# Optimization experiments

Measured on AMD Instinct MI355X. Metric: run time of the kernel, lower is better.

## Reference

```python
import jax, jax.numpy as jnp
import numpy as np

B, N, C_IN, C_OUT, D, K = 64, 2048, 32, 32, 16, 2


def setup_inputs() -> dict:
    key = jax.random.key(0)
    k1, k2, k3, k4 = jax.random.split(key, 4)
    x = jax.random.normal(k1, (B, N, C_IN), dtype=jnp.float32)
    node_embeddings = jax.random.normal(k2, (N, D), dtype=jnp.float32)
    weights_pool = jax.random.normal(k3, (D, K, C_IN, C_OUT), dtype=jnp.float32)
    bias_pool = jax.random.normal(k4, (D, C_OUT), dtype=jnp.float32)
    return {"x": x, "node_embeddings": node_embeddings,
            "weights_pool": weights_pool, "bias_pool": bias_pool}


def reference(x, node_embeddings, weights_pool, bias_pool):
    n = node_embeddings.shape[0]
    # adaptive adjacency: softmax(relu(E E^T), axis=1)  [N, N]
    supports = jax.nn.softmax(jax.nn.relu(node_embeddings @ node_embeddings.T), axis=1)
    # stack [I, A]  -> [K=2, N, N]
    supports = jnp.stack([jnp.eye(n, dtype=supports.dtype), supports], axis=0)
    # per-node weights [N, K, C_in, C_out] and bias [N, C_out]
    weights = jnp.einsum('nd,dkio->nkio', node_embeddings, weights_pool)
    bias = node_embeddings @ bias_pool
    # graph aggregation: [K,N,N] x [B,N,C] -> [B,N,K,C]
    x_g = jnp.einsum('knm,bmc->bnkc', supports, x)
    # per-node batched small GEMM: [B,N,K,Ci] x [N,K,Ci,Co] -> [B,N,Co]
    x_gconv = jnp.einsum('bnki,nkio->bno', x_g, weights) + bias
    return x_gconv
```

## Files before the change

### kernel.cpp

```cpp
#include <hip/hip_runtime.h>


#define NN 2048
#define NB 64
#define CI 32
#define CO 32
#define DD 16

typedef __attribute__((ext_vector_type(8))) short bf16x8;
typedef __attribute__((ext_vector_type(4))) float f32x4;

__device__ __forceinline__ unsigned short f2bf(float f) {
    unsigned u = __float_as_uint(f);
    u += 0x7FFF + ((u >> 16) & 1);
    return (unsigned short)(u >> 16);
}
__device__ __forceinline__ float bf2f(unsigned short h) {
    return __uint_as_float(((unsigned)h) << 16);
}

#define GLOAD16(gp, lp) __builtin_amdgcn_global_load_lds(                 \
    (const __attribute__((address_space(1))) void*)(gp),                  \
    (__attribute__((address_space(3))) void*)(lp), 16, 0, 0)

__global__ __launch_bounds__(256) void xT_kernel(const float* __restrict__ x,
                                                 unsigned short* __restrict__ xT)
{
    const int b = blockIdx.y;
    const int m0 = blockIdx.x * 64;
    const int tid = threadIdx.x;
    __shared__ float tile[64][33];
    #pragma unroll
    for (int k = 0; k < 2; ++k) {
        const int idx = tid + k * 256;
        const int r = idx >> 3, q = idx & 7;
        float4 v = *(const float4*)&x[((size_t)b * NN + m0 + r) * CI + q * 4];
        tile[r][q * 4 + 0] = v.x; tile[r][q * 4 + 1] = v.y;
        tile[r][q * 4 + 2] = v.z; tile[r][q * 4 + 3] = v.w;
    }
    __syncthreads();
    const int c = tid >> 3, m8 = (tid & 7) * 8;
    unsigned short o[8];
    #pragma unroll
    for (int e = 0; e < 8; ++e) o[e] = f2bf(tile[m8 + e][c]);
    *(uint4*)&xT[((size_t)b * CI + c) * NN + m0 + m8] = *(uint4*)o;
}

__global__ __launch_bounds__(256) void adj_kernel(const float* __restrict__ E,
                                                  unsigned short* __restrict__ Ahi,
                                                  unsigned short* __restrict__ Alo)
{
    const int n = blockIdx.x;
    const int tid = threadIdx.x;
    __shared__ float row[NN];
    __shared__ float redmax[4];
    __shared__ float redsum[4];

    const float4* __restrict__ E4 = reinterpret_cast<const float4*>(E);
    const float4 e0 = E4[n * 4 + 0], e1 = E4[n * 4 + 1];
    const float4 e2 = E4[n * 4 + 2], e3 = E4[n * 4 + 3];

    float lmax = 0.0f;
    #pragma unroll
    for (int k = 0; k < NN / 256; ++k) {
        const int m = tid + k * 256;
        const float4 f0 = E4[m * 4 + 0], f1 = E4[m * 4 + 1];
        const float4 f2 = E4[m * 4 + 2], f3 = E4[m * 4 + 3];
        float dot = e0.x * f0.x + e0.y * f0.y + e0.z * f0.z + e0.w * f0.w;
        dot += e1.x * f1.x + e1.y * f1.y + e1.z * f1.z + e1.w * f1.w;
        dot += e2.x * f2.x + e2.y * f2.y + e2.z * f2.z + e2.w * f2.w;
        dot += e3.x * f3.x + e3.y * f3.y + e3.z * f3.z + e3.w * f3.w;
        dot = fmaxf(dot, 0.0f);
        row[m] = dot;
        lmax = fmaxf(lmax, dot);
    }
    #pragma unroll
    for (int off = 32; off > 0; off >>= 1)
        lmax = fmaxf(lmax, __shfl_down(lmax, off, 64));
    if ((tid & 63) == 0) redmax[tid >> 6] = lmax;
    __syncthreads();
    const float gmax = fmaxf(fmaxf(redmax[0], redmax[1]), fmaxf(redmax[2], redmax[3]));

    float lsum = 0.0f;
    #pragma unroll
    for (int k = 0; k < NN / 256; ++k) {
        const int m = tid + k * 256;
        const float v = __expf(row[m] - gmax);
        row[m] = v;
        lsum += v;
    }
    #pragma unroll
    for (int off = 32; off > 0; off >>= 1)
        lsum += __shfl_down(lsum, off, 64);
    if ((tid & 63) == 0) redsum[tid >> 6] = lsum;
    __syncthreads();
    const float inv = 1.0f / (redsum[0] + redsum[1] + redsum[2] + redsum[3]);

    #pragma unroll
    for (int k = 0; k < NN / 256; ++k) {
        const int m = tid + k * 256;
        const float a = row[m] * inv;
        const unsigned short h = f2bf(a);
        Ahi[(size_t)n * NN + m] = h;
        Alo[(size_t)n * NN + m] = f2bf(a - bf2f(h));
    }
}

__global__ __launch_bounds__(256, 2) void agg_mfma(const unsigned short* __restrict__ Ahi,
                                                   const unsigned short* __restrict__ Alo,
                                                   const unsigned short* __restrict__ xT,
                                                   float* __restrict__ agg)
{
    const int n0 = blockIdx.y * 64;
    const int j0 = blockIdx.x * 128;
    const int tid = threadIdx.x;
    const int lane = tid & 63;
    const int w = tid >> 6;
    const int wr = w >> 1, wc = w & 1;

    __shared__ __align__(16) unsigned char sm[65536];

    int soffA[2]; size_t gA[2];
    #pragma unroll
    for (int i = 0; i < 2; ++i) {
        const int off = i * 4096 + tid * 16;
        const int row = off >> 7, cb = off & 127;
        const int mm = (cb ^ ((row & 7) << 4)) >> 1;
        soffA[i] = off;
        gA[i] = (size_t)(n0 + row) * NN + mm;
    }
    int soffX[4]; size_t gX[4];
    #pragma unroll
    for (int i = 0; i < 4; ++i) {
        const int off = i * 4096 + tid * 16;
        const int row = off >> 7, cb = off & 127;
        const int mm = (cb ^ ((row & 7) << 4)) >> 1;
        soffX[i] = 16384 + off;
        gX[i] = (size_t)(j0 + row) * NN + mm;
    }

    const int l15 = lane & 15, lk = lane >> 4;
    const int sw = (lane & 7) << 4;
    int cbs[2];
    cbs[0] = (lk << 4) ^ sw;
    cbs[1] = (64 + (lk << 4)) ^ sw;
    int offA[2][2], offL[2][2], offX[4][2];
    #pragma unroll
    for (int fm = 0; fm < 2; ++fm) {
        const int r = wr * 32 + fm * 16 + l15;
        #pragma unroll
        for (int s = 0; s < 2; ++s) {
            offA[fm][s] = (r << 7) + cbs[s];
            offL[fm][s] = 8192 + (r << 7) + cbs[s];
        }
    }
    #pragma unroll
    for (int fj = 0; fj < 4; ++fj) {
        const int r = wc * 64 + fj * 16 + l15;
        #pragma unroll
        for (int s = 0; s < 2; ++s)
            offX[fj][s] = 16384 + (r << 7) + cbs[s];
    }

    f32x4 acc[2][4];
    #pragma unroll
    for (int fm = 0; fm < 2; ++fm)
        #pragma unroll
        for (int fj = 0; fj < 4; ++fj) acc[fm][fj] = (f32x4)0.0f;

    #pragma unroll
    for (int i = 0; i < 2; ++i) {
        GLOAD16(Ahi + gA[i], sm + soffA[i]);
        GLOAD16(Alo + gA[i], sm + 8192 + soffA[i]);
    }
    #pragma unroll
    for (int i = 0; i < 4; ++i)
        GLOAD16(xT + gX[i], sm + soffX[i]);
    __syncthreads();

    int buf = 0;
    for (int ks = 0; ks < NN / 64; ++ks) {
        const int nb = buf ^ 1;
        if (ks != NN / 64 - 1) {
            const size_t adv = (size_t)(ks + 1) * 64;
            #pragma unroll
            for (int i = 0; i < 2; ++i) {
                GLOAD16(Ahi + gA[i] + adv, sm + nb * 32768 + soffA[i]);
                GLOAD16(Alo + gA[i] + adv, sm + nb * 32768 + 8192 + soffA[i]);
            }
            #pragma unroll
            for (int i = 0; i < 4; ++i)
                GLOAD16(xT + gX[i] + adv, sm + nb * 32768 + soffX[i]);
        }
        const unsigned char* Bp = sm + buf * 32768;
        bf16x8 av[2][2], lv[2][2], xv[4][2];
        #pragma unroll
        for (int fm = 0; fm < 2; ++fm)
            #pragma unroll
            for (int s = 0; s < 2; ++s) {
                av[fm][s] = *(const bf16x8*)(Bp + offA[fm][s]);
                lv[fm][s] = *(const bf16x8*)(Bp + offL[fm][s]);
            }
        #pragma unroll
        for (int fj = 0; fj < 4; ++fj)
            #pragma unroll
            for (int s = 0; s < 2; ++s)
                xv[fj][s] = *(const bf16x8*)(Bp + offX[fj][s]);

        #pragma unroll
        for (int s = 0; s < 2; ++s)
            #pragma unroll
            for (int fm = 0; fm < 2; ++fm)
                #pragma unroll
                for (int fj = 0; fj < 4; ++fj) {
                    acc[fm][fj] = __builtin_amdgcn_mfma_f32_16x16x32_bf16(
                        av[fm][s], xv[fj][s], acc[fm][fj], 0, 0, 0);
                    acc[fm][fj] = __builtin_amdgcn_mfma_f32_16x16x32_bf16(
                        lv[fm][s], xv[fj][s], acc[fm][fj], 0, 0, 0);
                }
        __syncthreads();
        buf = nb;
    }

    #pragma unroll
    for (int fm = 0; fm < 2; ++fm)
        #pragma unroll
        for (int fj = 0; fj < 4; ++fj) {
            const int nbase = n0 + wr * 32 + fm * 16 + lk * 4;
            const int j = j0 + wc * 64 + fj * 16 + l15;
            const int b = j >> 5, c = j & 31;
            #pragma unroll
            for (int r = 0; r < 4; ++r)
                agg[((size_t)b * NN + nbase + r) * CI + c] = acc[fm][fj][r];
        }
}

__global__ __launch_bounds__(256) void wgen_kernel(const float* __restrict__ E,
                                                   const float* __restrict__ Wp,
                                                   float* __restrict__ Wfull)
{
    const int n0 = blockIdx.x * 4;
    const int tid = threadIdx.x;
    __shared__ float e[4][16];
    if (tid < 64) e[tid >> 4][tid & 15] = E[(n0 + (tid >> 4)) * DD + (tid & 15)];
    __syncthreads();

    const float4* __restrict__ Wp4 = (const float4*)Wp;
    float4 a0[4], a1[4];
    #pragma unroll
    for (int g = 0; g < 4; ++g) {
        a0[g] = make_float4(0.f, 0.f, 0.f, 0.f);
        a1[g] = make_float4(0.f, 0.f, 0.f, 0.f);
    }
    #pragma unroll
    for (int d = 0; d < DD; ++d) {
        const float4 w0 = Wp4[d * 512 + tid];
        const float4 w1 = Wp4[d * 512 + 256 + tid];
        #pragma unroll
        for (int g = 0; g < 4; ++g) {
            const float c = e[g][d];
            a0[g].x = fmaf(c, w0.x, a0[g].x); a0[g].y = fmaf(c, w0.y, a0[g].y);
            a0[g].z = fmaf(c, w0.z, a0[g].z); a0[g].w = fmaf(c, w0.w, a0[g].w);
            a1[g].x = fmaf(c, w1.x, a1[g].x); a1[g].y = fmaf(c, w1.y, a1[g].y);
            a1[g].z = fmaf(c, w1.z, a1[g].z); a1[g].w = fmaf(c, w1.w, a1[g].w);
        }
    }
    float4* __restrict__ O4 = (float4*)Wfull;
    #pragma unroll
    for (int g = 0; g < 4; ++g) {
        O4[(size_t)(n0 + g) * 512 + tid]       = a0[g];
        O4[(size_t)(n0 + g) * 512 + 256 + tid] = a1[g];
    }
}

__global__ __launch_bounds__(256) void out_kernel(const float* __restrict__ E,
                                                  const float* __restrict__ Bp,
                                                  const float* __restrict__ x,
                                                  const float* __restrict__ Wfull,
                                                  float* __restrict__ out)
{
    const int n = blockIdx.x;
    const int tid = threadIdx.x;

    __shared__ __align__(16) float W[2 * CI * CO];
    __shared__ __align__(16) float Xs[NB][CI];
    __shared__ __align__(16) float Gs[NB][CI];
    __shared__ float e[DD];

    {
        const float* Wsrc = Wfull + (size_t)n * 2048;
        GLOAD16(Wsrc + tid * 4,        (char*)W + tid * 16);
        GLOAD16(Wsrc + 1024 + tid * 4, (char*)W + 4096 + tid * 16);
        const int b = tid >> 3, q = (tid & 7) * 4;
        const int b2 = (tid + 256) >> 3, q2 = (tid & 7) * 4;
        GLOAD16(x + ((size_t)b * NN + n) * CI + q,    (char*)Xs + tid * 16);
        GLOAD16(x + ((size_t)b2 * NN + n) * CI + q2,  (char*)Xs + 4096 + tid * 16);
        GLOAD16(out + ((size_t)b * NN + n) * CI + q,  (char*)Gs + tid * 16);
        GLOAD16(out + ((size_t)b2 * NN + n) * CI + q2,(char*)Gs + 4096 + tid * 16);
    }
    if (tid < DD) e[tid] = E[n * DD + tid];
    __syncthreads();

    const int o  = tid & 31;
    const int bb = tid >> 5;

    float bias = 0.0f;
    #pragma unroll
    for (int d = 0; d < DD; ++d) bias = fmaf(e[d], Bp[d * CO + o], bias);

    float w0[CI], w1[CI];
    #pragma unroll
    for (int i = 0; i < CI; ++i) {
        w0[i] = W[i * 32 + o];
        w1[i] = W[1024 + i * 32 + o];
    }

    #pragma unroll
    for (int j = 0; j < 8; ++j) {
        const int b = bb + 8 * j;
        float s = bias;
        #pragma unroll
        for (int iq = 0; iq < 8; ++iq) {
            const float4 xq = *(const float4*)&Xs[b][iq * 4];
            const float4 gq = *(const float4*)&Gs[b][iq * 4];
            s = fmaf(xq.x, w0[iq * 4 + 0], s);
            s = fmaf(xq.y, w0[iq * 4 + 1], s);
            s = fmaf(xq.z, w0[iq * 4 + 2], s);
            s = fmaf(xq.w, w0[iq * 4 + 3], s);
            s = fmaf(gq.x, w1[iq * 4 + 0], s);
            s = fmaf(gq.y, w1[iq * 4 + 1], s);
            s = fmaf(gq.z, w1[iq * 4 + 2], s);
            s = fmaf(gq.w, w1[iq * 4 + 3], s);
        }
        out[((size_t)b * NN + n) * CO + o] = s;
    }
}

extern "C" void kernel_launch(void* const* d_in, const int* in_sizes, int n_in,
                              void* d_out, int out_size, void* d_ws, size_t ws_size,
                              hipStream_t stream)
{
    const float* x  = (const float*)d_in[0];
    const float* E  = (const float*)d_in[1];
    const float* Wp = (const float*)d_in[2];
    const float* Bp = (const float*)d_in[3];
    float* out = (float*)d_out;

    unsigned short* Ahi = (unsigned short*)d_ws;
    unsigned short* Alo = Ahi + (size_t)NN * NN;
    unsigned short* xT  = Alo + (size_t)NN * NN;
    float* Wfull = (float*)d_ws;

    xT_kernel<<<dim3(NN / 64, NB), 256, 0, stream>>>(x, xT);
    adj_kernel<<<NN, 256, 0, stream>>>(E, Ahi, Alo);
    agg_mfma<<<dim3(NN / 128, NN / 64), 256, 0, stream>>>(Ahi, Alo, xT, out);
    wgen_kernel<<<NN / 4, 256, 0, stream>>>(E, Wp, Wfull);
    out_kernel<<<NN, 256, 0, stream>>>(E, Bp, x, Wfull, out);
}
```

Measured before the change: 159.5 us.

## Fuse xT transpose into adjacency kernel and weight generation into output kernel

Merges the x-transpose-to-bf16 kernel into the adjacency softmax kernel, since both launch 2048 blocks and can share the grid. It also computes the per-node weights inside the output kernel directly into LDS instead of writing and rereading an 8 MB Wfull buffer. This removes two kernel launches and a global round trip. In exchange, each output block now reads the full 128 KB weights_pool through cache, and the adjacency kernel uses more shared memory.

```diff
diff --git a/kernel.cpp b/kernel.cpp
--- a/kernel.cpp
+++ b/kernel.cpp
@@ -23,38 +23,38 @@
     (const __attribute__((address_space(1))) void*)(gp),                  \
     (__attribute__((address_space(3))) void*)(lp), 16, 0, 0)
 
-__global__ __launch_bounds__(256) void xT_kernel(const float* __restrict__ x,
-                                                 unsigned short* __restrict__ xT)
-{
-    const int b = blockIdx.y;
-    const int m0 = blockIdx.x * 64;
-    const int tid = threadIdx.x;
-    __shared__ float tile[64][33];
-    #pragma unroll
-    for (int k = 0; k < 2; ++k) {
-        const int idx = tid + k * 256;
-        const int r = idx >> 3, q = idx & 7;
-        float4 v = *(const float4*)&x[((size_t)b * NN + m0 + r) * CI + q * 4];
-        tile[r][q * 4 + 0] = v.x; tile[r][q * 4 + 1] = v.y;
-        tile[r][q * 4 + 2] = v.z; tile[r][q * 4 + 3] = v.w;
-    }
-    __syncthreads();
-    const int c = tid >> 3, m8 = (tid & 7) * 8;
-    unsigned short o[8];
-    #pragma unroll
-    for (int e = 0; e < 8; ++e) o[e] = f2bf(tile[m8 + e][c]);
-    *(uint4*)&xT[((size_t)b * CI + c) * NN + m0 + m8] = *(uint4*)o;
-}
-
-__global__ __launch_bounds__(256) void adj_kernel(const float* __restrict__ E,
-                                                  unsigned short* __restrict__ Ahi,
-                                                  unsigned short* __restrict__ Alo)
+__global__ __launch_bounds__(256) void adjxT_kernel(const float* __restrict__ E,
+                                                    const float* __restrict__ x,
+                                                    unsigned short* __restrict__ Ahi,
+                                                    unsigned short* __restrict__ Alo,
+                                                    unsigned short* __restrict__ xT)
 {
     const int n = blockIdx.x;
     const int tid = threadIdx.x;
+
+    __shared__ float tile[64][33];
     __shared__ float row[NN];
     __shared__ float redmax[4];
     __shared__ float redsum[4];
+
+    {
+        const int b = n >> 5;
+        const int m0 = (n & 31) * 64;
+        #pragma unroll
+        for (int k = 0; k < 2; ++k) {
+            const int idx = tid + k * 256;
+            const int r = idx >> 3, q = idx & 7;
+            float4 v = *(const float4*)&x[((size_t)b * NN + m0 + r) * CI + q * 4];
+            tile[r][q * 4 + 0] = v.x; tile[r][q * 4 + 1] = v.y;
+            tile[r][q * 4 + 2] = v.z; tile[r][q * 4 + 3] = v.w;
+        }
+        __syncthreads();
+        const int c = tid >> 3, m8 = (tid & 7) * 8;
+        unsigned short o[8];
+        #pragma unroll
+        for (int e = 0; e < 8; ++e) o[e] = f2bf(tile[m8 + e][c]);
+        *(uint4*)&xT[((size_t)b * CI + c) * NN + m0 + m8] = *(uint4*)o;
+    }
 
     const float4* __restrict__ E4 = reinterpret_cast<const float4*>(E);
     const float4 e0 = E4[n * 4 + 0], e1 = E4[n * 4 + 1];
@@ -235,49 +235,11 @@
         }
 }
 
-__global__ __launch_bounds__(256) void wgen_kernel(const float* __restrict__ E,
+__global__ __launch_bounds__(256) void outw_kernel(const float* __restrict__ E,
                                                    const float* __restrict__ Wp,
-                                                   float* __restrict__ Wfull)
-{
-    const int n0 = blockIdx.x * 4;
-    const int tid = threadIdx.x;
-    __shared__ float e[4][16];
-    if (tid < 64) e[tid >> 4][tid & 15] = E[(n0 + (tid >> 4)) * DD + (tid & 15)];
-    __syncthreads();
-
-    const float4* __restrict__ Wp4 = (const float4*)Wp;
-    float4 a0[4], a1[4];
-    #pragma unroll
-    for (int g = 0; g < 4; ++g) {
-        a0[g] = make_float4(0.f, 0.f, 0.f, 0.f);
-        a1[g] = make_float4(0.f, 0.f, 0.f, 0.f);
-    }
-    #pragma unroll
-    for (int d = 0; d < DD; ++d) {
-        const float4 w0 = Wp4[d * 512 + tid];
-        const float4 w1 = Wp4[d * 512 + 256 + tid];
-        #pragma unroll
-        for (int g = 0; g < 4; ++g) {
-            const float c = e[g][d];
-            a0[g].x = fmaf(c, w0.x, a0[g].x); a0[g].y = fmaf(c, w0.y, a0[g].y);
-            a0[g].z = fmaf(c, w0.z, a0[g].z); a0[g].w = fmaf(c, w0.w, a0[g].w);
-            a1[g].x = fmaf(c, w1.x, a1[g].x); a1[g].y = fmaf(c, w1.y, a1[g].y);
-            a1[g].z = fmaf(c, w1.z, a1[g].z); a1[g].w = fmaf(c, w1.w, a1[g].w);
-        }
-    }
-    float4* __restrict__ O4 = (float4*)Wfull;
-    #pragma unroll
-    for (int g = 0; g < 4; ++g) {
-        O4[(size_t)(n0 + g) * 512 + tid]       = a0[g];
-        O4[(size_t)(n0 + g) * 512 + 256 + tid] = a1[g];
-    }
-}
-
-__global__ __launch_bounds__(256) void out_kernel(const float* __restrict__ E,
-                                                  const float* __restrict__ Bp,
-                                                  const float* __restrict__ x,
-                                                  const float* __restrict__ Wfull,
-                                                  float* __restrict__ out)
+                                                   const float* __restrict__ Bp,
+                                                   const float* __restrict__ x,
+                                                   float* __restrict__ out)
 {
     const int n = blockIdx.x;
     const int tid = threadIdx.x;
@@ -285,20 +247,37 @@
     __shared__ __align__(16) float W[2 * CI * CO];
     __shared__ __align__(16) float Xs[NB][CI];
     __shared__ __align__(16) float Gs[NB][CI];
-    __shared__ float e[DD];
 
     {
-        const float* Wsrc = Wfull + (size_t)n * 2048;
-        GLOAD16(Wsrc + tid * 4,        (char*)W + tid * 16);
-        GLOAD16(Wsrc + 1024 + tid * 4, (char*)W + 4096 + tid * 16);
         const int b = tid >> 3, q = (tid & 7) * 4;
-        const int b2 = (tid + 256) >> 3, q2 = (tid & 7) * 4;
-        GLOAD16(x + ((size_t)b * NN + n) * CI + q,    (char*)Xs + tid * 16);
-        GLOAD16(x + ((size_t)b2 * NN + n) * CI + q2,  (char*)Xs + 4096 + tid * 16);
-        GLOAD16(out + ((size_t)b * NN + n) * CI + q,  (char*)Gs + tid * 16);
-        GLOAD16(out + ((size_t)b2 * NN + n) * CI + q2,(char*)Gs + 4096 + tid * 16);
-    }
-    if (tid < DD) e[tid] = E[n * DD + tid];
+        const int b2 = (tid + 256) >> 3;
+        GLOAD16(x + ((size_t)b * NN + n) * CI + q,     (char*)Xs + tid * 16);
+        GLOAD16(x + ((size_t)b2 * NN + n) * CI + q,    (char*)Xs + 4096 + tid * 16);
+        GLOAD16(out + ((size_t)b * NN + n) * CI + q,   (char*)Gs + tid * 16);
+        GLOAD16(out + ((size_t)b2 * NN + n) * CI + q,  (char*)Gs + 4096 + tid * 16);
+    }
+
+    float e[DD];
+    #pragma unroll
+    for (int d = 0; d < DD; ++d) e[d] = E[n * DD + d];
+
+    {
+        const float4* __restrict__ Wp4 = (const float4*)Wp;
+        float4 a0 = make_float4(0.f, 0.f, 0.f, 0.f);
+        float4 a1 = make_float4(0.f, 0.f, 0.f, 0.f);
+        #pragma unroll
+        for (int d = 0; d < DD; ++d) {
+            const float4 w0 = Wp4[d * 512 + tid];
+            const float4 w1 = Wp4[d * 512 + 256 + tid];
+            const float c = e[d];
+            a0.x = fmaf(c, w0.x, a0.x); a0.y = fmaf(c, w0.y, a0.y);
+            a0.z = fmaf(c, w0.z, a0.z); a0.w = fmaf(c, w0.w, a0.w);
+            a1.x = fmaf(c, w1.x, a1.x); a1.y = fmaf(c, w1.y, a1.y);
+            a1.z = fmaf(c, w1.z, a1.z); a1.w = fmaf(c, w1.w, a1.w);
+        }
+        *(float4*)&W[tid * 4] = a0;
+        *(float4*)&W[1024 + tid * 4] = a1;
+    }
     __syncthreads();
 
     const int o  = tid & 31;
@@ -349,11 +328,8 @@
     unsigned short* Ahi = (unsigned short*)d_ws;
     unsigned short* Alo = Ahi + (size_t)NN * NN;
     unsigned short* xT  = Alo + (size_t)NN * NN;
-    float* Wfull = (float*)d_ws;
-
-    xT_kernel<<<dim3(NN / 64, NB), 256, 0, stream>>>(x, xT);
-    adj_kernel<<<NN, 256, 0, stream>>>(E, Ahi, Alo);
+
+    adjxT_kernel<<<NN, 256, 0, stream>>>(E, x, Ahi, Alo, xT);
     agg_mfma<<<dim3(NN / 128, NN / 64), 256, 0, stream>>>(Ahi, Alo, xT, out);
-    wgen_kernel<<<NN / 4, 256, 0, stream>>>(E, Wp, Wfull);
-    out_kernel<<<NN, 256, 0, stream>>>(E, Bp, x, Wfull, out);
-}
+    outw_kernel<<<NN, 256, 0, stream>>>(E, Wp, Bp, x, out);
+}
```

Result: faster. 144.2 us (-9.6%).
